# Kernel optimization log

Hardware: AMD Instinct MI355X
Metric: run time of the kernel (lower is better)

Reference implementation:

```python
import jax, jax.numpy as jnp
import numpy as np

B, N, E, H = 4, 2048, 1024, 16
D = E // H  # head dim = 64


def setup_inputs() -> dict:
    key = jax.random.key(0)
    k1, k2, k3 = jax.random.split(key, 3)
    x = jax.random.normal(k1, (B, N, E), dtype=jnp.float32)
    # torch nn.Linear weights are [out_features, in_features]
    w_qkv = jax.random.normal(k2, (3 * E, E), dtype=jnp.float32) * (E ** -0.5)
    w_out = jax.random.normal(k3, (E, E), dtype=jnp.float32) * (E ** -0.5)
    return {"x": x, "w_qkv": w_qkv, "w_out": w_out}


def reference(x, w_qkv, w_out):
    # fused QKV projection: [B,N,E] @ [E,3E] -> [B,N,3E]
    qkv = jnp.einsum("bne,fe->bnf", x, w_qkv)
    q, k, v = jnp.split(qkv, 3, axis=-1)
    # b n (h d) -> b h n d
    split_heads = lambda t: t.reshape(B, N, H, D).transpose(0, 2, 1, 3)
    q, k, v = map(split_heads, (q, k, v))
    scale = D ** -0.5
    scores = jnp.einsum("bhnd,bhmd->bhnm", q, k) * scale
    attn = jax.nn.softmax(scores, axis=-1)
    out = jnp.einsum("bhnm,bhmd->bhnd", attn, v)
    # b h n d -> b n (h d)
    out = out.transpose(0, 2, 1, 3).reshape(B, N, E)
    return jnp.einsum("bne,fe->bnf", out, w_out)
```

## Files before the change

kernel.cpp:

```cpp
#include <hip/hip_runtime.h>
#include <hip/hip_bf16.h>

typedef short bf16x8 __attribute__((ext_vector_type(8)));
typedef float f32x4 __attribute__((ext_vector_type(4)));
using bf16 = __hip_bfloat16;

#define MFMA16(a, b, c) __builtin_amdgcn_mfma_f32_16x16x32_bf16(a, b, c, 0, 0, 0)

typedef unsigned int u32;
typedef u32 __attribute__((address_space(1))) global_u32;
typedef u32 __attribute__((address_space(3))) lds_u32;

__device__ __forceinline__ void gload_lds16(const unsigned short* g, unsigned short* l) {
    __builtin_amdgcn_global_load_lds((const global_u32*)g, (lds_u32*)l, 16, 0, 0);
}

__device__ __forceinline__ short f2b(float f) {
    __hip_bfloat16 h = __float2bfloat16(f);
    return *reinterpret_cast<short*>(&h);
}

__global__ __launch_bounds__(256) void cvt_kernel(const float* __restrict__ src,
                                                  unsigned short* __restrict__ dst) {
    const size_t i = ((size_t)blockIdx.x * 256 + threadIdx.x) * 8;
    float4 v0 = *(const float4*)(src + i);
    float4 v1 = *(const float4*)(src + i + 4);
    bf16x8 o;
    o[0] = f2b(v0.x); o[1] = f2b(v0.y); o[2] = f2b(v0.z); o[3] = f2b(v0.w);
    o[4] = f2b(v1.x); o[5] = f2b(v1.y); o[6] = f2b(v1.z); o[7] = f2b(v1.w);
    *(bf16x8*)(dst + i) = o;
}

template <int MODE>
__global__ __launch_bounds__(256) void gemm128_kernel(const unsigned short* __restrict__ A,
                                                      const unsigned short* __restrict__ W,
                                                      void* __restrict__ outp) {
    __shared__ unsigned short As[128][64];
    __shared__ unsigned short Ws[128][64];
    const int tid = threadIdx.x;
    const int lane = tid & 63;
    const int w = tid >> 6;
    const int wr = w >> 1, wc = w & 1;
    const int lm = lane & 15, quad = lane >> 4;
    const int m0 = blockIdx.y * 128, n0 = blockIdx.x * 128;

    const int srow8 = lane >> 3;
    const int skg = (lane & 7) ^ srow8;
    const unsigned short* Ag = A + (size_t)(m0 + w * 32 + srow8) * 1024 + skg * 8;
    const unsigned short* Wg = W + (size_t)(n0 + w * 32 + srow8) * 1024 + skg * 8;

    f32x4 acc[4][4] = {};

    for (int k0 = 0; k0 < 1024; k0 += 64) {
        __syncthreads();
#pragma unroll
        for (int j = 0; j < 4; j++) {
            gload_lds16(Ag + j * (8 * 1024), &As[w * 32 + j * 8][0]);
            gload_lds16(Wg + j * (8 * 1024), &Ws[w * 32 + j * 8][0]);
        }
        Ag += 64;
        Wg += 64;
        __syncthreads();
#pragma unroll
        for (int ks = 0; ks < 2; ks++) {
            const int swz = ((quad + ks * 4) ^ (lm & 7)) * 8;
            bf16x8 af[4], bf[4];
#pragma unroll
            for (int mt = 0; mt < 4; mt++)
                af[mt] = *(const bf16x8*)&As[wr * 64 + mt * 16 + lm][swz];
#pragma unroll
            for (int nt = 0; nt < 4; nt++)
                bf[nt] = *(const bf16x8*)&Ws[wc * 64 + nt * 16 + lm][swz];
#pragma unroll
            for (int mt = 0; mt < 4; mt++)
#pragma unroll
                for (int nt = 0; nt < 4; nt++)
                    acc[mt][nt] = MFMA16(af[mt], bf[nt], acc[mt][nt]);
        }
    }

#pragma unroll
    for (int mt = 0; mt < 4; mt++)
#pragma unroll
        for (int nt = 0; nt < 4; nt++) {
            f32x4 v = acc[mt][nt];
            const int gr0 = m0 + wr * 64 + mt * 16 + quad * 4;
            const int gc = n0 + wc * 64 + nt * 16 + lm;
            if (MODE == 2) {
                bf16* qkv = (bf16*)outp;
                const int which = gc >> 10;
                const int h = (gc >> 6) & 15;
                const int d = gc & 63;
                const int b = gr0 >> 11, n = gr0 & 2047;
                if (which == 2) {
                    short4 pk;
                    pk.x = f2b(v[0]); pk.y = f2b(v[1]); pk.z = f2b(v[2]); pk.w = f2b(v[3]);
                    *(short4*)&qkv[2ull * 8388608 +
                                   ((size_t)((b * 16 + h) * 64 + d)) * 2048 + n] = pk;
                } else {
#pragma unroll
                    for (int r = 0; r < 4; r++) {
                        float val = v[r];
                        if (which == 0) val *= 0.125f;
                        qkv[(size_t)which * 8388608 +
                            ((size_t)((b * 16 + h) * 2048 + n + r)) * 64 + d] =
                            __float2bfloat16(val);
                    }
                }
            } else {
                float* o = (float*)outp;
#pragma unroll
                for (int r = 0; r < 4; r++) o[(size_t)(gr0 + r) * 1024 + gc] = v[r];
            }
        }
}

__global__ __launch_bounds__(256, 4) void attn_mfma_kernel(
    const unsigned short* __restrict__ Qg, const unsigned short* __restrict__ Kg,
    const unsigned short* __restrict__ Vtg, unsigned short* __restrict__ O) {
    __shared__ short Ks[64][72];
    __shared__ short Vs[64][72];
    __shared__ short Ps[4][2][16][72];
    const int tid = threadIdx.x;
    const int lane = tid & 63;
    const int w = tid >> 6;
    const int lm = lane & 15;
    const int quad = lane >> 4;
    const int bh = blockIdx.y;
    const int n0 = blockIdx.x * 128;
    const size_t base = (size_t)bh * (2048 * 64);

    bf16x8 qf[2][2];
#pragma unroll
    for (int mt = 0; mt < 2; mt++)
#pragma unroll
        for (int ks = 0; ks < 2; ks++)
            qf[mt][ks] = *(const bf16x8*)&Qg[base +
                                            (size_t)(n0 + w * 32 + mt * 16 + lm) * 64 +
                                            ks * 32 + quad * 8];

    f32x4 accO[2][4] = {};
    float lst[2] = {0.f, 0.f};

    const int srow = tid >> 2, scol = (tid & 3) * 16;

    for (int t = 0; t < 32; t++) {
        const int k0 = t * 64;
        const unsigned short* kp = &Kg[base + (size_t)(k0 + srow) * 64 + scol];
        bf16x8 ka0 = *(const bf16x8*)kp;
        bf16x8 ka1 = *(const bf16x8*)(kp + 8);
        const unsigned short* vp = &Vtg[base + (size_t)srow * 2048 + k0 + scol];
        bf16x8 va0 = *(const bf16x8*)vp;
        bf16x8 va1 = *(const bf16x8*)(vp + 8);
        __syncthreads();
        *(bf16x8*)&Ks[srow][scol] = ka0;
        *(bf16x8*)&Ks[srow][scol + 8] = ka1;
        *(bf16x8*)&Vs[srow][scol] = va0;
        *(bf16x8*)&Vs[srow][scol + 8] = va1;
        __syncthreads();

        bf16x8 kb[4][2];
#pragma unroll
        for (int kt = 0; kt < 4; kt++)
#pragma unroll
            for (int ks = 0; ks < 2; ks++)
                kb[kt][ks] = *(const bf16x8*)&Ks[kt * 16 + lm][ks * 32 + quad * 8];
        f32x4 s[2][4];
#pragma unroll
        for (int mt = 0; mt < 2; mt++)
#pragma unroll
            for (int kt = 0; kt < 4; kt++) {
                f32x4 z = {};
                z = MFMA16(kb[kt][0], qf[mt][0], z);
                s[mt][kt] = MFMA16(kb[kt][1], qf[mt][1], z);
            }

#pragma unroll
        for (int mt = 0; mt < 2; mt++) {
            float ps = 0.f;
#pragma unroll
            for (int kt = 0; kt < 4; kt++) {
                const float p0 = __expf(s[mt][kt][0]);
                const float p1 = __expf(s[mt][kt][1]);
                const float p2 = __expf(s[mt][kt][2]);
                const float p3 = __expf(s[mt][kt][3]);
                ps += (p0 + p1) + (p2 + p3);
                short4 pk;
                pk.x = f2b(p0); pk.y = f2b(p1); pk.z = f2b(p2); pk.w = f2b(p3);
                *(short4*)&Ps[w][mt][lm][kt * 16 + quad * 4] = pk;
            }
            lst[mt] += ps;
        }

        bf16x8 vbf[4][2];
#pragma unroll
        for (int nt = 0; nt < 4; nt++)
#pragma unroll
            for (int ks = 0; ks < 2; ks++)
                vbf[nt][ks] = *(const bf16x8*)&Vs[nt * 16 + lm][ks * 32 + quad * 8];
#pragma unroll
        for (int mt = 0; mt < 2; mt++) {
            bf16x8 pb0 = *(const bf16x8*)&Ps[w][mt][lm][quad * 8];
            bf16x8 pb1 = *(const bf16x8*)&Ps[w][mt][lm][32 + quad * 8];
#pragma unroll
            for (int nt = 0; nt < 4; nt++) {
                f32x4 a = MFMA16(vbf[nt][0], pb0, accO[mt][nt]);
                accO[mt][nt] = MFMA16(vbf[nt][1], pb1, a);
            }
        }
    }

#pragma unroll
    for (int mt = 0; mt < 2; mt++) {
        lst[mt] += __shfl_xor(lst[mt], 16);
        lst[mt] += __shfl_xor(lst[mt], 32);
    }

    const int b = bh >> 4, h = bh & 15;
#pragma unroll
    for (int mt = 0; mt < 2; mt++) {
        const float inv = 1.0f / lst[mt];
        const int n = n0 + w * 32 + mt * 16 + lm;
#pragma unroll
        for (int nt = 0; nt < 4; nt++) {
            short4 pk;
            pk.x = f2b(accO[mt][nt][0] * inv);
            pk.y = f2b(accO[mt][nt][1] * inv);
            pk.z = f2b(accO[mt][nt][2] * inv);
            pk.w = f2b(accO[mt][nt][3] * inv);
            *(short4*)&O[((size_t)(b * 2048 + n)) * 1024 + h * 64 + nt * 16 + quad * 4] = pk;
        }
    }
}

extern "C" void kernel_launch(void* const* d_in, const int* in_sizes, int n_in,
                              void* d_out, int out_size, void* d_ws, size_t ws_size,
                              hipStream_t stream) {
    const float* x = (const float*)d_in[0];
    const float* w_qkv = (const float*)d_in[1];
    const float* w_out = (const float*)d_in[2];
    float* out = (float*)d_out;

    unsigned short* qkvb = (unsigned short*)d_ws;
    unsigned short* xb = qkvb + 3ull * 8388608;
    unsigned short* wqkvb = xb + 8388608;
    unsigned short* woutb = wqkvb + 3145728;

    cvt_kernel<<<4096, 256, 0, stream>>>(x, xb);
    cvt_kernel<<<1536, 256, 0, stream>>>(w_qkv, wqkvb);
    cvt_kernel<<<512, 256, 0, stream>>>(w_out, woutb);
    gemm128_kernel<2><<<dim3(24, 64), 256, 0, stream>>>(xb, wqkvb, (void*)qkvb);
    attn_mfma_kernel<<<dim3(16, 64), 256, 0, stream>>>(qkvb, qkvb + 8388608,
                                                       qkvb + 2 * 8388608, xb);
    gemm128_kernel<1><<<dim3(8, 64), 256, 0, stream>>>(xb, woutb, out);
}
```

Baseline: 282.9 us.

## Use direct global-to-LDS loads with XOR swizzle in attention, merge convert launches

```diff
diff --git a/kernel.cpp b/kernel.cpp
--- a/kernel.cpp
+++ b/kernel.cpp
@@ -20,9 +20,24 @@
     return *reinterpret_cast<short*>(&h);
 }
 
-__global__ __launch_bounds__(256) void cvt_kernel(const float* __restrict__ src,
-                                                  unsigned short* __restrict__ dst) {
-    const size_t i = ((size_t)blockIdx.x * 256 + threadIdx.x) * 8;
+__global__ __launch_bounds__(256) void cvt3_kernel(const float* __restrict__ x,
+                                                   const float* __restrict__ wq,
+                                                   const float* __restrict__ wo,
+                                                   unsigned short* __restrict__ xb,
+                                                   unsigned short* __restrict__ wqb,
+                                                   unsigned short* __restrict__ wob) {
+    const int id = blockIdx.x;
+    const float* src;
+    unsigned short* dst;
+    size_t off;
+    if (id < 4096) {
+        src = x; dst = xb; off = (size_t)id * 2048;
+    } else if (id < 5632) {
+        src = wq; dst = wqb; off = (size_t)(id - 4096) * 2048;
+    } else {
+        src = wo; dst = wob; off = (size_t)(id - 5632) * 2048;
+    }
+    const size_t i = off + (size_t)threadIdx.x * 8;
     float4 v0 = *(const float4*)(src + i);
     float4 v1 = *(const float4*)(src + i + 4);
     bf16x8 o;
@@ -118,16 +133,16 @@
 __global__ __launch_bounds__(256, 4) void attn_mfma_kernel(
     const unsigned short* __restrict__ Qg, const unsigned short* __restrict__ Kg,
     const unsigned short* __restrict__ Vtg, unsigned short* __restrict__ O) {
-    __shared__ short Ks[64][72];
-    __shared__ short Vs[64][72];
-    __shared__ short Ps[4][2][16][72];
+    __shared__ unsigned short Ks[64][64];
+    __shared__ unsigned short Vs[64][64];
+    __shared__ unsigned short Ps[4][2][16][64];
     const int tid = threadIdx.x;
     const int lane = tid & 63;
     const int w = tid >> 6;
     const int lm = lane & 15;
     const int quad = lane >> 4;
-    const int bh = blockIdx.y;
-    const int n0 = blockIdx.x * 128;
+    const int bh = blockIdx.x & 63;
+    const int n0 = (blockIdx.x >> 6) * 128;
     const size_t base = (size_t)bh * (2048 * 64);
 
     bf16x8 qf[2][2];
@@ -142,21 +157,18 @@
     f32x4 accO[2][4] = {};
     float lst[2] = {0.f, 0.f};
 
-    const int srow = tid >> 2, scol = (tid & 3) * 16;
+    const int sr = lane >> 3;
+    const int sg = (lane & 7) ^ sr;
 
     for (int t = 0; t < 32; t++) {
         const int k0 = t * 64;
-        const unsigned short* kp = &Kg[base + (size_t)(k0 + srow) * 64 + scol];
-        bf16x8 ka0 = *(const bf16x8*)kp;
-        bf16x8 ka1 = *(const bf16x8*)(kp + 8);
-        const unsigned short* vp = &Vtg[base + (size_t)srow * 2048 + k0 + scol];
-        bf16x8 va0 = *(const bf16x8*)vp;
-        bf16x8 va1 = *(const bf16x8*)(vp + 8);
-        __syncthreads();
-        *(bf16x8*)&Ks[srow][scol] = ka0;
-        *(bf16x8*)&Ks[srow][scol + 8] = ka1;
-        *(bf16x8*)&Vs[srow][scol] = va0;
-        *(bf16x8*)&Vs[srow][scol + 8] = va1;
+        __syncthreads();
+#pragma unroll
+        for (int j = 0; j < 2; j++) {
+            const int row = w * 16 + j * 8 + sr;
+            gload_lds16(&Kg[base + (size_t)(k0 + row) * 64 + sg * 8], &Ks[w * 16 + j * 8][0]);
+            gload_lds16(&Vtg[base + (size_t)row * 2048 + k0 + sg * 8], &Vs[w * 16 + j * 8][0]);
+        }
         __syncthreads();
 
         bf16x8 kb[4][2];
@@ -164,7 +176,8 @@
         for (int kt = 0; kt < 4; kt++)
 #pragma unroll
             for (int ks = 0; ks < 2; ks++)
-                kb[kt][ks] = *(const bf16x8*)&Ks[kt * 16 + lm][ks * 32 + quad * 8];
+                kb[kt][ks] = *(const bf16x8*)&Ks[kt * 16 + lm]
+                                               [(((ks * 4 + quad) ^ (lm & 7)) * 8)];
         f32x4 s[2][4];
 #pragma unroll
         for (int mt = 0; mt < 2; mt++)
@@ -187,7 +200,8 @@
                 ps += (p0 + p1) + (p2 + p3);
                 short4 pk;
                 pk.x = f2b(p0); pk.y = f2b(p1); pk.z = f2b(p2); pk.w = f2b(p3);
-                *(short4*)&Ps[w][mt][lm][kt * 16 + quad * 4] = pk;
+                const int g = kt * 2 + (quad >> 1);
+                *(short4*)&Ps[w][mt][lm][((g ^ (lm & 7)) * 8) + (quad & 1) * 4] = pk;
             }
             lst[mt] += ps;
         }
@@ -197,11 +211,12 @@
         for (int nt = 0; nt < 4; nt++)
 #pragma unroll
             for (int ks = 0; ks < 2; ks++)
-                vbf[nt][ks] = *(const bf16x8*)&Vs[nt * 16 + lm][ks * 32 + quad * 8];
+                vbf[nt][ks] = *(const bf16x8*)&Vs[nt * 16 + lm]
+                                                [(((ks * 4 + quad) ^ (lm & 7)) * 8)];
 #pragma unroll
         for (int mt = 0; mt < 2; mt++) {
-            bf16x8 pb0 = *(const bf16x8*)&Ps[w][mt][lm][quad * 8];
-            bf16x8 pb1 = *(const bf16x8*)&Ps[w][mt][lm][32 + quad * 8];
+            bf16x8 pb0 = *(const bf16x8*)&Ps[w][mt][lm][(((quad) ^ (lm & 7)) * 8)];
+            bf16x8 pb1 = *(const bf16x8*)&Ps[w][mt][lm][(((4 + quad) ^ (lm & 7)) * 8)];
 #pragma unroll
             for (int nt = 0; nt < 4; nt++) {
                 f32x4 a = MFMA16(vbf[nt][0], pb0, accO[mt][nt]);
@@ -246,11 +261,9 @@
     unsigned short* wqkvb = xb + 8388608;
     unsigned short* woutb = wqkvb + 3145728;
 
-    cvt_kernel<<<4096, 256, 0, stream>>>(x, xb);
-    cvt_kernel<<<1536, 256, 0, stream>>>(w_qkv, wqkvb);
-    cvt_kernel<<<512, 256, 0, stream>>>(w_out, woutb);
+    cvt3_kernel<<<6144, 256, 0, stream>>>(x, w_qkv, w_out, xb, wqkvb, woutb);
     gemm128_kernel<2><<<dim3(24, 64), 256, 0, stream>>>(xb, wqkvb, (void*)qkvb);
-    attn_mfma_kernel<<<dim3(16, 64), 256, 0, stream>>>(qkvb, qkvb + 8388608,
-                                                       qkvb + 2 * 8388608, xb);
+    attn_mfma_kernel<<<1024, 256, 0, stream>>>(qkvb, qkvb + 8388608,
+                                               qkvb + 2 * 8388608, xb);
     gemm128_kernel<1><<<dim3(8, 64), 256, 0, stream>>>(xb, woutb, out);
 }
```

New measurement: 262.1 us. 7.4% less time.
